# Kernel optimization log

Measured on AMD Instinct MI355X. Metric: run time of the kernel, lower is better.

## Reference

```python
import jax, jax.numpy as jnp
import numpy as np

N_NODES = 50000
N_EDGES = 819200  # divisible by num_rels=8 -> equal relation segments (implicit rel_ptr)
NUM_RELS = 8
N_HEADS = 4
IN_FEAT = 256
OUT_FEAT = 128
HEAD_DIM = OUT_FEAT // N_HEADS
LEAKY_SLOPE = 0.2


def setup_inputs() -> dict:
    key = jax.random.key(0)
    ks = jax.random.split(key, 7)
    inputs = jax.random.normal(ks[0], (N_NODES, IN_FEAT), dtype=jnp.float32)
    conv_weights = jax.random.normal(ks[1], (NUM_RELS, N_HEADS, IN_FEAT, HEAD_DIM), dtype=jnp.float32) * (1.0 / np.sqrt(IN_FEAT))
    attn_l = jax.random.normal(ks[2], (NUM_RELS, N_HEADS, HEAD_DIM), dtype=jnp.float32) * 0.1
    attn_r = jax.random.normal(ks[3], (NUM_RELS, N_HEADS, HEAD_DIM), dtype=jnp.float32) * 0.1
    h_bias = jax.random.normal(ks[4], (OUT_FEAT,), dtype=jnp.float32) * 0.01
    row_idx = jax.random.randint(ks[5], (N_EDGES,), 0, N_NODES, dtype=jnp.int32)
    col_idx = jax.random.randint(ks[6], (N_EDGES,), 0, N_NODES, dtype=jnp.int32)
    return {
        'inputs': inputs,
        'conv_weights': conv_weights,
        'attn_l': attn_l,
        'attn_r': attn_r,
        'h_bias': h_bias,
        'row_idx': row_idx,
        'col_idx': col_idx,
    }


def reference(inputs, conv_weights, attn_l, attn_r, h_bias, row_idx, col_idx):
    R, H, IN, D = conv_weights.shape
    E = row_idx.shape[0]
    N = inputs.shape[0]
    epr = E // R  # edges per relation (equal segments == rel_ptr)

    # relation-grouped GEMM: per-edge transformed src features [R, epr, H, D]
    src = inputs[row_idx].reshape(R, epr, IN)
    feat_src = jnp.einsum('rei,rhid->rehd', src, conv_weights)
    el = jnp.einsum('rehd,rhd->reh', feat_src, attn_l)

    dst = inputs[col_idx].reshape(R, epr, IN)
    feat_dst = jnp.einsum('rei,rhid->rehd', dst, conv_weights)
    er = jnp.einsum('rehd,rhd->reh', feat_dst, attn_r)

    # fused GAT: leaky_relu(el+er), softmax over incoming edges per dst node
    e = jax.nn.leaky_relu((el + er).reshape(E, H), negative_slope=LEAKY_SLOPE)
    m = jax.ops.segment_max(e, col_idx, num_segments=N)          # [N, H]
    e_exp = jnp.exp(e - m[col_idx])                              # [E, H]
    denom = jax.ops.segment_sum(e_exp, col_idx, num_segments=N)  # [N, H]
    alpha = e_exp / denom[col_idx]                               # [E, H]

    feat = feat_src.reshape(E, H, D)
    h = jax.ops.segment_sum(alpha[:, :, None] * feat, col_idx, num_segments=N)  # [N, H, D]
    h = h.reshape(N, H * D) + h_bias
    # activation=None, self_loop=False, dropout treated as eval (identity)
    return h
```

## Files before the change

### kernel.cpp

```cpp
#include <hip/hip_runtime.h>
#include <hip/hip_bf16.h>

#define N_NODES 50000
#define N_EDGES 819200
#define NUM_RELS 8
#define EPR (N_EDGES / NUM_RELS)
#define N_HEADS 4
#define IN_FEAT 256
#define OUT_FEAT 128
#define HEAD_DIM 32
#define NB_SCAN ((N_NODES + 255) / 256)

typedef __attribute__((ext_vector_type(8))) __bf16 bf16x8;
typedef __attribute__((ext_vector_type(4))) __bf16 bf16x4;
typedef __attribute__((ext_vector_type(4))) float f32x4;

#define SZ_FEAT ((size_t)NUM_RELS * N_NODES * OUT_FEAT)
#define SZ_EL ((size_t)NUM_RELS * N_NODES * N_HEADS)
#define SZ_WB ((size_t)IN_FEAT * 64)
#define SZ_WT ((size_t)NUM_RELS * OUT_FEAT * IN_FEAT / 2)
#define OFF_FEAT ((size_t)0)
#define OFF_EL (OFF_FEAT + SZ_FEAT)
#define OFF_ER (OFF_EL + SZ_EL)
#define OFF_WB (OFF_ER + SZ_EL)
#define OFF_WT (OFF_WB + SZ_WB)
#define OFF_INT (OFF_WT + SZ_WT)
#define IOFF_CNT ((size_t)0)
#define IOFF_PTR ((size_t)N_NODES)
#define IOFF_CUR ((size_t)2 * N_NODES)
#define IOFF_BSUM ((size_t)3 * N_NODES)
#define IOFF_SPAY ((size_t)3 * N_NODES + 256)

__global__ void k_cvtw(const float* __restrict__ cw, __bf16* __restrict__ wtg) {
    int tid = blockIdx.x * blockDim.x + threadIdx.x;
    if (tid >= 32768) return;
    int oct = tid & 3, brow = (tid >> 2) & 127, ks = (tid >> 9) & 1, kc = (tid >> 10) & 3, r = tid >> 12;
    int k0 = kc * 64 + ks * 32 + oct * 8;
    int h = brow >> 5, d = brow & 31;
    const float* src = cw + ((size_t)(r * N_HEADS + h) * IN_FEAT + k0) * HEAD_DIM + d;
    bf16x8 v;
#pragma unroll
    for (int j = 0; j < 8; ++j) v[j] = (__bf16)src[j * HEAD_DIM];
    *(bf16x8*)(wtg + (size_t)tid * 8) = v;
}

__global__ void k_wboth(const float* __restrict__ cw, const float* __restrict__ al,
                        const float* __restrict__ ar, __bf16* __restrict__ wbt) {
    int tid = blockIdx.x * blockDim.x + threadIdx.x;
    if (tid >= IN_FEAT * 64) return;
    int col = tid >> 8, i = tid & 255;
    int side = col >> 5, r = (col >> 2) & 7, h = col & 3;
    const float* av = (side ? ar : al) + (size_t)(r * N_HEADS + h) * HEAD_DIM;
    const float* cwp = cw + ((size_t)(r * N_HEADS + h) * IN_FEAT + i) * HEAD_DIM;
    float s = 0.f;
#pragma unroll
    for (int d = 0; d < HEAD_DIM; ++d) s += cwp[d] * av[d];
    wbt[(size_t)col * IN_FEAT + i] = (__bf16)s;
}

__global__ void k_wbg(const __bf16* __restrict__ wbt, __bf16* __restrict__ wbg) {
    int tid = blockIdx.x * blockDim.x + threadIdx.x;
    if (tid >= 2048) return;
    int oct = tid & 3, brow = (tid >> 2) & 63, ks = (tid >> 8) & 1, kc = tid >> 9;
    int k0 = kc * 64 + ks * 32 + oct * 8;
    bf16x8 v = *(const bf16x8*)(wbt + (size_t)brow * IN_FEAT + k0);
    *(bf16x8*)(wbg + (size_t)tid * 8) = v;
}

__device__ __forceinline__ void loadB(bf16x8 (&dst)[8], const __bf16* __restrict__ wtg,
                                      int r, int kc, int wc, int lane) {
#pragma unroll
    for (int ks = 0; ks < 2; ++ks)
#pragma unroll
        for (int cb = 0; cb < 4; ++cb)
            dst[ks * 4 + cb] = *(const bf16x8*)(wtg +
                ((size_t)((((r * 4 + kc) * 2 + ks) * 128) + wc * 64 + cb * 16 + (lane & 15)) * 4 + (lane >> 4)) * 8);
}

__device__ __forceinline__ void loadB2(bf16x8 (&dst)[4], const __bf16* __restrict__ wbg,
                                       int kc, int wc, int lane) {
#pragma unroll
    for (int ks = 0; ks < 2; ++ks)
#pragma unroll
        for (int cb = 0; cb < 2; ++cb)
            dst[ks * 2 + cb] = *(const bf16x8*)(wbg +
                ((size_t)(((kc * 2 + ks) * 64) + wc * 32 + cb * 16 + (lane & 15)) * 4 + (lane >> 4)) * 8);
}

__device__ __forceinline__ void compK(f32x4 (&acc)[4][4], const unsigned char* sA,
                                      const bf16x8 (&bg)[8], int kc, int wr, int lane) {
#pragma unroll
    for (int ks = 0; ks < 2; ++ks) {
        bf16x8 af[4];
#pragma unroll
        for (int rb = 0; rb < 4; ++rb) {
            int rowa = wr * 64 + rb * 16 + (lane & 15);
            int slot = kc * 8 + ((ks * 4 + (lane >> 4)) ^ (rowa & 7));
            af[rb] = *(const bf16x8*)(sA + rowa * 512 + slot * 16);
        }
#pragma unroll
        for (int rb = 0; rb < 4; ++rb)
#pragma unroll
            for (int cb = 0; cb < 4; ++cb)
                acc[rb][cb] = __builtin_amdgcn_mfma_f32_16x16x32_bf16(af[rb], bg[ks * 4 + cb], acc[rb][cb], 0, 0, 0);
    }
}

__device__ __forceinline__ void compK2(f32x4 (&acc2)[4][2], const unsigned char* sA,
                                       const bf16x8 (&bg)[4], int kc, int wr, int lane) {
#pragma unroll
    for (int ks = 0; ks < 2; ++ks) {
        bf16x8 af[4];
#pragma unroll
        for (int rb = 0; rb < 4; ++rb) {
            int rowa = wr * 64 + rb * 16 + (lane & 15);
            int slot = kc * 8 + ((ks * 4 + (lane >> 4)) ^ (rowa & 7));
            af[rb] = *(const bf16x8*)(sA + rowa * 512 + slot * 16);
        }
#pragma unroll
        for (int rb = 0; rb < 4; ++rb)
#pragma unroll
            for (int cb = 0; cb < 2; ++cb)
                acc2[rb][cb] = __builtin_amdgcn_mfma_f32_16x16x32_bf16(af[rb], bg[ks * 2 + cb], acc2[rb][cb], 0, 0, 0);
    }
}

__global__ __launch_bounds__(256) void k_fused(const float* __restrict__ x,
                                               const __bf16* __restrict__ wtg,
                                               const __bf16* __restrict__ wbg,
                                               __bf16* __restrict__ featb,
                                               float* __restrict__ el,
                                               float* __restrict__ er) {
    __shared__ __align__(16) unsigned char sA[65536];
    const int t = threadIdx.x, lane = t & 63, w = t >> 6;
    const int wr = w >> 1, wc = w & 1;
    const int n0 = blockIdx.x * 128;

#pragma unroll 8
    for (int i = 0; i < 32; ++i) {
        int flat = i * 256 + t;
        int row = flat >> 6;
        int kq = flat & 63;
        int n = n0 + row;
        if (n >= N_NODES) n = N_NODES - 1;
        float4 v = *(const float4*)(x + (size_t)n * IN_FEAT + kq * 4);
        bf16x4 hv;
        hv[0] = (__bf16)v.x; hv[1] = (__bf16)v.y; hv[2] = (__bf16)v.z; hv[3] = (__bf16)v.w;
        int sg = kq >> 1;
        int slot = (sg & ~7) | ((sg & 7) ^ (row & 7));
        *(bf16x4*)(sA + row * 512 + slot * 16 + (kq & 1) * 8) = hv;
    }
    __syncthreads();

    bf16x8 bgA[8], bgB[8];
    for (int r = 0; r < NUM_RELS; ++r) {
        f32x4 acc[4][4];
#pragma unroll
        for (int i = 0; i < 4; ++i)
#pragma unroll
            for (int j = 0; j < 4; ++j) acc[i][j] = (f32x4){0.f, 0.f, 0.f, 0.f};

        loadB(bgA, wtg, r, 0, wc, lane);
        loadB(bgB, wtg, r, 1, wc, lane);
        compK(acc, sA, bgA, 0, wr, lane);
        loadB(bgA, wtg, r, 2, wc, lane);
        compK(acc, sA, bgB, 1, wr, lane);
        loadB(bgB, wtg, r, 3, wc, lane);
        compK(acc, sA, bgA, 2, wr, lane);
        compK(acc, sA, bgB, 3, wr, lane);

#pragma unroll
        for (int rb = 0; rb < 4; ++rb)
#pragma unroll
            for (int q = 0; q < 4; ++q) {
                int rowi = wr * 64 + rb * 16 + (lane >> 4) * 4 + q;
                int n = n0 + rowi;
                if (n < N_NODES) {
                    __bf16* fp = featb + ((size_t)r * N_NODES + n) * OUT_FEAT + wc * 64 + (lane & 15);
#pragma unroll
                    for (int cb = 0; cb < 4; ++cb) fp[cb * 16] = (__bf16)acc[rb][cb][q];
                }
            }
    }

    f32x4 acc2[4][2];
#pragma unroll
    for (int i = 0; i < 4; ++i)
#pragma unroll
        for (int j = 0; j < 2; ++j) acc2[i][j] = (f32x4){0.f, 0.f, 0.f, 0.f};

    bf16x8 cgA[4], cgB[4];
    loadB2(cgA, wbg, 0, wc, lane);
    loadB2(cgB, wbg, 1, wc, lane);
    compK2(acc2, sA, cgA, 0, wr, lane);
    loadB2(cgA, wbg, 2, wc, lane);
    compK2(acc2, sA, cgB, 1, wr, lane);
    loadB2(cgB, wbg, 3, wc, lane);
    compK2(acc2, sA, cgA, 2, wr, lane);
    compK2(acc2, sA, cgB, 3, wr, lane);

#pragma unroll
    for (int rb = 0; rb < 4; ++rb)
#pragma unroll
        for (int q = 0; q < 4; ++q) {
            int n = n0 + wr * 64 + rb * 16 + (lane >> 4) * 4 + q;
            if (n < N_NODES) {
#pragma unroll
                for (int cb = 0; cb < 2; ++cb) {
                    int c = wc * 32 + cb * 16 + (lane & 15);
                    int side = c >> 5, rr = (c >> 2) & 7, h = c & 3;
                    float* dst = side ? er : el;
                    dst[((size_t)rr * N_NODES + n) * N_HEADS + h] = acc2[rb][cb][q];
                }
            }
        }
}

__global__ void k_hist(const int* __restrict__ col, int* __restrict__ cnt) {
    int e = blockIdx.x * blockDim.x + threadIdx.x;
    if (e < N_EDGES) atomicAdd(cnt + col[e], 1);
}

__global__ __launch_bounds__(256) void k_scanA(const int* __restrict__ cnt,
                                               int* __restrict__ excl,
                                               int* __restrict__ bsum) {
    __shared__ int s[256];
    int i = blockIdx.x * 256 + threadIdx.x;
    int v = (i < N_NODES) ? cnt[i] : 0;
    s[threadIdx.x] = v;
    __syncthreads();
#pragma unroll
    for (int off = 1; off < 256; off <<= 1) {
        int t = (threadIdx.x >= off) ? s[threadIdx.x - off] : 0;
        __syncthreads();
        s[threadIdx.x] += t;
        __syncthreads();
    }
    if (i < N_NODES) excl[i] = s[threadIdx.x] - v;
    if (threadIdx.x == 255) bsum[blockIdx.x] = s[255];
}

__global__ __launch_bounds__(256) void k_scanB(int* __restrict__ bsum) {
    __shared__ int s[256];
    int v = (threadIdx.x < NB_SCAN) ? bsum[threadIdx.x] : 0;
    s[threadIdx.x] = v;
    __syncthreads();
#pragma unroll
    for (int off = 1; off < 256; off <<= 1) {
        int t = (threadIdx.x >= off) ? s[threadIdx.x - off] : 0;
        __syncthreads();
        s[threadIdx.x] += t;
        __syncthreads();
    }
    bsum[threadIdx.x] = s[threadIdx.x] - v;
}

__global__ __launch_bounds__(256) void k_scanC(int* __restrict__ ptr,
                                               int* __restrict__ cursor,
                                               const int* __restrict__ bsum) {
    int i = blockIdx.x * 256 + threadIdx.x;
    if (i >= N_NODES) return;
    int p = ptr[i] + bsum[blockIdx.x];
    ptr[i] = p;
    cursor[i] = p;
}

__global__ void k_scatter(const int* __restrict__ row, const int* __restrict__ col,
                          int* __restrict__ cursor, int* __restrict__ spay) {
    int e = blockIdx.x * blockDim.x + threadIdx.x;
    if (e >= N_EDGES) return;
    int c = col[e];
    int pos = atomicAdd(cursor + c, 1);
    spay[pos] = row[e] | ((e / EPR) << 20);
}

__global__ __launch_bounds__(256) void k_agg(const int* __restrict__ ptr,
                                             const int* __restrict__ cnt,
                                             const int* __restrict__ spay,
                                             const float* __restrict__ el,
                                             const float* __restrict__ er,
                                             const __bf16* __restrict__ featb,
                                             const float* __restrict__ bias,
                                             float* __restrict__ out) {
    const int wv = threadIdx.x >> 6, lane = threadIdx.x & 63;
    const int n = blockIdx.x * 4 + wv;
    if (n >= N_NODES) return;
    const int start = ptr[n], len = cnt[n];
    const int h = lane >> 4;
    float accx = 0.f, accy = 0.f, den = 0.f;
    int j = 0;
    for (; j + 4 <= len; j += 4) {
        int p[4];
#pragma unroll
        for (int u = 0; u < 4; ++u) p[u] = spay[start + j + u];
        float w[4], vx[4], vy[4];
#pragma unroll
        for (int u = 0; u < 4; ++u) {
            int rw = p[u] & 0xFFFFF, r = p[u] >> 20;
            size_t rb = (size_t)r * N_NODES;
            float s = el[(rb + rw) * N_HEADS + h] + er[(rb + n) * N_HEADS + h];
            s = s > 0.f ? s : 0.2f * s;
            w[u] = __expf(s);
            ushort2 raw = *(const ushort2*)(featb + (rb + rw) * OUT_FEAT + lane * 2);
            vx[u] = __uint_as_float((unsigned)raw.x << 16);
            vy[u] = __uint_as_float((unsigned)raw.y << 16);
        }
#pragma unroll
        for (int u = 0; u < 4; ++u) {
            accx += w[u] * vx[u];
            accy += w[u] * vy[u];
            den += w[u];
        }
    }
    for (; j < len; ++j) {
        int p = spay[start + j];
        int rw = p & 0xFFFFF, r = p >> 20;
        size_t rb = (size_t)r * N_NODES;
        float s = el[(rb + rw) * N_HEADS + h] + er[(rb + n) * N_HEADS + h];
        s = s > 0.f ? s : 0.2f * s;
        float w = __expf(s);
        ushort2 raw = *(const ushort2*)(featb + (rb + rw) * OUT_FEAT + lane * 2);
        accx += w * __uint_as_float((unsigned)raw.x << 16);
        accy += w * __uint_as_float((unsigned)raw.y << 16);
        den += w;
    }
    float inv = (len > 0) ? 1.f / den : 0.f;
    int o = lane * 2;
    float2 res;
    res.x = accx * inv + bias[o];
    res.y = accy * inv + bias[o + 1];
    *(float2*)(out + (size_t)n * OUT_FEAT + o) = res;
}

extern "C" void kernel_launch(void* const* d_in, const int* in_sizes, int n_in,
                              void* d_out, int out_size, void* d_ws, size_t ws_size,
                              hipStream_t stream) {
    const float* x = (const float*)d_in[0];
    const float* cw = (const float*)d_in[1];
    const float* al = (const float*)d_in[2];
    const float* ar = (const float*)d_in[3];
    const float* bias = (const float*)d_in[4];
    const int* row = (const int*)d_in[5];
    const int* col = (const int*)d_in[6];
    float* out = (float*)d_out;
    float* ws = (float*)d_ws;

    __bf16* featb = (__bf16*)(ws + OFF_FEAT);
    float* el = ws + OFF_EL;
    float* er = ws + OFF_ER;
    __bf16* wbt = (__bf16*)(ws + OFF_WB);
    __bf16* wbg = (__bf16*)(ws + OFF_WB + 8192);
    __bf16* wtg = (__bf16*)(ws + OFF_WT);
    int* iw = (int*)(ws + OFF_INT);
    int* cnt = iw + IOFF_CNT;
    int* ptr = iw + IOFF_PTR;
    int* cur = iw + IOFF_CUR;
    int* bsum = iw + IOFF_BSUM;
    int* spay = iw + IOFF_SPAY;

    hipMemsetAsync(cnt, 0, N_NODES * sizeof(int), stream);

    k_cvtw<<<128, 256, 0, stream>>>(cw, wtg);
    k_wboth<<<(IN_FEAT * 64 + 255) / 256, 256, 0, stream>>>(cw, al, ar, wbt);
    k_wbg<<<8, 256, 0, stream>>>(wbt, wbg);
    k_fused<<<(N_NODES + 127) / 128, 256, 0, stream>>>(x, wtg, wbg, featb, el, er);

    k_hist<<<(N_EDGES + 255) / 256, 256, 0, stream>>>(col, cnt);
    k_scanA<<<NB_SCAN, 256, 0, stream>>>(cnt, ptr, bsum);
    k_scanB<<<1, 256, 0, stream>>>(bsum);
    k_scanC<<<NB_SCAN, 256, 0, stream>>>(ptr, cur, bsum);
    k_scatter<<<(N_EDGES + 255) / 256, 256, 0, stream>>>(row, col, cur, spay);

    k_agg<<<(N_NODES + 3) / 4, 256, 0, stream>>>(ptr, cnt, spay, el, er, featb, bias, out);
}
```

Before: 240.4 us.

## Split fused GEMM across 16 waves with narrow 16-column tiles per wave

The node-transform GEMM kernel goes from 256-thread blocks, where each wave computes a 64x64 tile, to 1024-thread blocks with 16 waves, each computing a 64x16 tile. The el/er projection GEMM runs on only the first four column waves. The goal is more waves in flight to hide global weight loads and the scattered output stores, and fewer accumulator registers per wave. The cost is four times more LDS reads of the A operand per output, since each wave now reuses an A fragment for only one MFMA column block. The aggressive launch bounds hint (1024, 4) may also force register spills, and the 64KB of LDS per block already limits how many blocks fit on a CU.

```diff
diff --git a/kernel.cpp b/kernel.cpp
--- a/kernel.cpp
+++ b/kernel.cpp
@@ -67,28 +67,24 @@
     *(bf16x8*)(wbg + (size_t)tid * 8) = v;
 }
 
-__device__ __forceinline__ void loadB(bf16x8 (&dst)[8], const __bf16* __restrict__ wtg,
+__device__ __forceinline__ void loadB(bf16x8 (&dst)[2], const __bf16* __restrict__ wtg,
                                       int r, int kc, int wc, int lane) {
 #pragma unroll
     for (int ks = 0; ks < 2; ++ks)
-#pragma unroll
-        for (int cb = 0; cb < 4; ++cb)
-            dst[ks * 4 + cb] = *(const bf16x8*)(wtg +
-                ((size_t)((((r * 4 + kc) * 2 + ks) * 128) + wc * 64 + cb * 16 + (lane & 15)) * 4 + (lane >> 4)) * 8);
-}
-
-__device__ __forceinline__ void loadB2(bf16x8 (&dst)[4], const __bf16* __restrict__ wbg,
-                                       int kc, int wc, int lane) {
+        dst[ks] = *(const bf16x8*)(wtg +
+            ((size_t)((((r * 4 + kc) * 2 + ks) * 128) + wc * 16 + (lane & 15)) * 4 + (lane >> 4)) * 8);
+}
+
+__device__ __forceinline__ void loadB2(bf16x8 (&dst)[2], const __bf16* __restrict__ wbg,
+                                       int wc, int kc, int lane) {
 #pragma unroll
     for (int ks = 0; ks < 2; ++ks)
-#pragma unroll
-        for (int cb = 0; cb < 2; ++cb)
-            dst[ks * 2 + cb] = *(const bf16x8*)(wbg +
-                ((size_t)(((kc * 2 + ks) * 64) + wc * 32 + cb * 16 + (lane & 15)) * 4 + (lane >> 4)) * 8);
-}
-
-__device__ __forceinline__ void compK(f32x4 (&acc)[4][4], const unsigned char* sA,
-                                      const bf16x8 (&bg)[8], int kc, int wr, int lane) {
+        dst[ks] = *(const bf16x8*)(wbg +
+            ((size_t)(((kc * 2 + ks) * 64) + wc * 16 + (lane & 15)) * 4 + (lane >> 4)) * 8);
+}
+
+__device__ __forceinline__ void compK(f32x4 (&acc)[4], const unsigned char* sA,
+                                      const bf16x8 (&bg)[2], int kc, int wr, int lane) {
 #pragma unroll
     for (int ks = 0; ks < 2; ++ks) {
         bf16x8 af[4];
@@ -100,45 +96,24 @@
         }
 #pragma unroll
         for (int rb = 0; rb < 4; ++rb)
-#pragma unroll
-            for (int cb = 0; cb < 4; ++cb)
-                acc[rb][cb] = __builtin_amdgcn_mfma_f32_16x16x32_bf16(af[rb], bg[ks * 4 + cb], acc[rb][cb], 0, 0, 0);
-    }
-}
-
-__device__ __forceinline__ void compK2(f32x4 (&acc2)[4][2], const unsigned char* sA,
-                                       const bf16x8 (&bg)[4], int kc, int wr, int lane) {
-#pragma unroll
-    for (int ks = 0; ks < 2; ++ks) {
-        bf16x8 af[4];
-#pragma unroll
-        for (int rb = 0; rb < 4; ++rb) {
-            int rowa = wr * 64 + rb * 16 + (lane & 15);
-            int slot = kc * 8 + ((ks * 4 + (lane >> 4)) ^ (rowa & 7));
-            af[rb] = *(const bf16x8*)(sA + rowa * 512 + slot * 16);
-        }
-#pragma unroll
-        for (int rb = 0; rb < 4; ++rb)
-#pragma unroll
-            for (int cb = 0; cb < 2; ++cb)
-                acc2[rb][cb] = __builtin_amdgcn_mfma_f32_16x16x32_bf16(af[rb], bg[ks * 2 + cb], acc2[rb][cb], 0, 0, 0);
-    }
-}
-
-__global__ __launch_bounds__(256) void k_fused(const float* __restrict__ x,
-                                               const __bf16* __restrict__ wtg,
-                                               const __bf16* __restrict__ wbg,
-                                               __bf16* __restrict__ featb,
-                                               float* __restrict__ el,
-                                               float* __restrict__ er) {
+            acc[rb] = __builtin_amdgcn_mfma_f32_16x16x32_bf16(af[rb], bg[ks], acc[rb], 0, 0, 0);
+    }
+}
+
+__global__ __launch_bounds__(1024, 4) void k_fused(const float* __restrict__ x,
+                                                   const __bf16* __restrict__ wtg,
+                                                   const __bf16* __restrict__ wbg,
+                                                   __bf16* __restrict__ featb,
+                                                   float* __restrict__ el,
+                                                   float* __restrict__ er) {
     __shared__ __align__(16) unsigned char sA[65536];
     const int t = threadIdx.x, lane = t & 63, w = t >> 6;
-    const int wr = w >> 1, wc = w & 1;
+    const int wr = w >> 3, wc = w & 7;
     const int n0 = blockIdx.x * 128;
 
-#pragma unroll 8
-    for (int i = 0; i < 32; ++i) {
-        int flat = i * 256 + t;
+#pragma unroll
+    for (int i = 0; i < 8; ++i) {
+        int flat = i * 1024 + t;
         int row = flat >> 6;
         int kq = flat & 63;
         int n = n0 + row;
@@ -152,13 +127,11 @@
     }
     __syncthreads();
 
-    bf16x8 bgA[8], bgB[8];
+    bf16x8 bgA[2], bgB[2];
     for (int r = 0; r < NUM_RELS; ++r) {
-        f32x4 acc[4][4];
-#pragma unroll
-        for (int i = 0; i < 4; ++i)
-#pragma unroll
-            for (int j = 0; j < 4; ++j) acc[i][j] = (f32x4){0.f, 0.f, 0.f, 0.f};
+        f32x4 acc[4];
+#pragma unroll
+        for (int i = 0; i < 4; ++i) acc[i] = (f32x4){0.f, 0.f, 0.f, 0.f};
 
         loadB(bgA, wtg, r, 0, wc, lane);
         loadB(bgB, wtg, r, 1, wc, lane);
@@ -175,45 +148,39 @@
             for (int q = 0; q < 4; ++q) {
                 int rowi = wr * 64 + rb * 16 + (lane >> 4) * 4 + q;
                 int n = n0 + rowi;
+                if (n < N_NODES)
+                    featb[((size_t)r * N_NODES + n) * OUT_FEAT + wc * 16 + (lane & 15)] =
+                        (__bf16)acc[rb][q];
+            }
+    }
+
+    if (wc < 4) {
+        f32x4 acc2[4];
+#pragma unroll
+        for (int i = 0; i < 4; ++i) acc2[i] = (f32x4){0.f, 0.f, 0.f, 0.f};
+        bf16x8 cgA[2], cgB[2];
+        loadB2(cgA, wbg, wc, 0, lane);
+        loadB2(cgB, wbg, wc, 1, lane);
+        compK(acc2, sA, cgA, 0, wr, lane);
+        loadB2(cgA, wbg, wc, 2, lane);
+        compK(acc2, sA, cgB, 1, wr, lane);
+        loadB2(cgB, wbg, wc, 3, lane);
+        compK(acc2, sA, cgA, 2, wr, lane);
+        compK(acc2, sA, cgB, 3, wr, lane);
+
+#pragma unroll
+        for (int rb = 0; rb < 4; ++rb)
+#pragma unroll
+            for (int q = 0; q < 4; ++q) {
+                int n = n0 + wr * 64 + rb * 16 + (lane >> 4) * 4 + q;
                 if (n < N_NODES) {
-                    __bf16* fp = featb + ((size_t)r * N_NODES + n) * OUT_FEAT + wc * 64 + (lane & 15);
-#pragma unroll
-                    for (int cb = 0; cb < 4; ++cb) fp[cb * 16] = (__bf16)acc[rb][cb][q];
+                    int c = wc * 16 + (lane & 15);
+                    int side = c >> 5, rr = (c >> 2) & 7, h = c & 3;
+                    float* dst = side ? er : el;
+                    dst[((size_t)rr * N_NODES + n) * N_HEADS + h] = acc2[rb][q];
                 }
             }
     }
-
-    f32x4 acc2[4][2];
-#pragma unroll
-    for (int i = 0; i < 4; ++i)
-#pragma unroll
-        for (int j = 0; j < 2; ++j) acc2[i][j] = (f32x4){0.f, 0.f, 0.f, 0.f};
-
-    bf16x8 cgA[4], cgB[4];
-    loadB2(cgA, wbg, 0, wc, lane);
-    loadB2(cgB, wbg, 1, wc, lane);
-    compK2(acc2, sA, cgA, 0, wr, lane);
-    loadB2(cgA, wbg, 2, wc, lane);
-    compK2(acc2, sA, cgB, 1, wr, lane);
-    loadB2(cgB, wbg, 3, wc, lane);
-    compK2(acc2, sA, cgA, 2, wr, lane);
-    compK2(acc2, sA, cgB, 3, wr, lane);
-
-#pragma unroll
-    for (int rb = 0; rb < 4; ++rb)
-#pragma unroll
-        for (int q = 0; q < 4; ++q) {
-            int n = n0 + wr * 64 + rb * 16 + (lane >> 4) * 4 + q;
-            if (n < N_NODES) {
-#pragma unroll
-                for (int cb = 0; cb < 2; ++cb) {
-                    int c = wc * 32 + cb * 16 + (lane & 15);
-                    int side = c >> 5, rr = (c >> 2) & 7, h = c & 3;
-                    float* dst = side ? er : el;
-                    dst[((size_t)rr * N_NODES + n) * N_HEADS + h] = acc2[rb][cb][q];
-                }
-            }
-        }
 }
 
 __global__ void k_hist(const int* __restrict__ col, int* __restrict__ cnt) {
@@ -363,7 +330,7 @@
     k_cvtw<<<128, 256, 0, stream>>>(cw, wtg);
     k_wboth<<<(IN_FEAT * 64 + 255) / 256, 256, 0, stream>>>(cw, al, ar, wbt);
     k_wbg<<<8, 256, 0, stream>>>(wbt, wbg);
-    k_fused<<<(N_NODES + 127) / 128, 256, 0, stream>>>(x, wtg, wbg, featb, el, er);
+    k_fused<<<(N_NODES + 127) / 128, 1024, 0, stream>>>(x, wtg, wbg, featb, el, er);
 
     k_hist<<<(N_EDGES + 255) / 256, 256, 0, stream>>>(col, cnt);
     k_scanA<<<NB_SCAN, 256, 0, stream>>>(cnt, ptr, bsum);
```

Result: slower. 321.9 us (+33.9%).
